# Optimization experiments

Measured on AMD Instinct MI355X. Metric: run time of the kernel, lower is better.

Reference implementation:

```python
import jax, jax.numpy as jnp
import numpy as np
from jax import lax


def setup_inputs() -> dict:
    key = jax.random.key(0)
    k1, k2 = jax.random.split(key)
    B, C, H, W = 4, 32, 512, 512
    x = jax.random.normal(k1, (B, C, H, W), dtype=jnp.float32)
    # offset conv params: out_ch = 2*k*k = 18 (init: small weights, zero bias)
    w_off = jax.random.normal(k2, (18, C, 3, 3), dtype=jnp.float32) * 0.05
    b_off = jnp.zeros((18,), dtype=jnp.float32)
    return {"x": x, "w_off": w_off, "b_off": b_off}


def _grid_sample_bilinear_zeros(x, grid):
    # x: (B,C,H,W); grid: (B,H,W,2) in [-1,1], align_corners=True, zeros padding
    B, C, H, W = x.shape
    ix = (grid[..., 0] + 1.0) * 0.5 * (W - 1)  # (B,H,W)
    iy = (grid[..., 1] + 1.0) * 0.5 * (H - 1)
    x0 = jnp.floor(ix); y0 = jnp.floor(iy)
    x1 = x0 + 1.0;      y1 = y0 + 1.0
    wx1 = ix - x0; wx0 = 1.0 - wx1
    wy1 = iy - y0; wy0 = 1.0 - wy1
    bi = jnp.arange(B)[:, None, None]

    def corner(yc, xc, w):
        valid = (xc >= 0) & (xc <= W - 1) & (yc >= 0) & (yc <= H - 1)
        xi = jnp.clip(xc, 0, W - 1).astype(jnp.int32)
        yi = jnp.clip(yc, 0, H - 1).astype(jnp.int32)
        v = x[bi, :, yi, xi]  # (B,H,W,C)
        return v * (w * valid.astype(x.dtype))[..., None]

    out = (corner(y0, x0, wy0 * wx0) + corner(y0, x1, wy0 * wx1)
           + corner(y1, x0, wy1 * wx0) + corner(y1, x1, wy1 * wx1))
    return out.transpose(0, 3, 1, 2)  # (B,C,H,W)


def reference(x, w_off, b_off):
    B, C, H, W = x.shape
    # offset conv: 3x3, stride 1, padding 1 (shape-preserving)
    off = lax.conv_general_dilated(
        x, w_off, window_strides=(1, 1), padding=((1, 1), (1, 1)),
        dimension_numbers=("NCHW", "OIHW", "NCHW"))
    off = off + b_off[None, :, None, None]               # (B,18,H,W)
    off = off.transpose(0, 2, 3, 1).reshape(B, H, W, 9, 2)
    # base integer grid: (x, y) per pixel
    gy, gx = jnp.meshgrid(jnp.arange(H, dtype=x.dtype),
                          jnp.arange(W, dtype=x.dtype), indexing="ij")
    base = jnp.stack([gx, gy], axis=-1)                  # (H,W,2)
    g = base[None, :, :, None, :] + off                  # (B,H,W,9,2)
    g = g / jnp.array([W - 1, H - 1], dtype=x.dtype) * 2.0 - 1.0
    g = g[:, :, :, 0, :]                                 # only first kernel offset used
    return _grid_sample_bilinear_zeros(x, g)
```

## Files before the change

### kernel.cpp

```cpp
#include <hip/hip_runtime.h>

#define BB 4
#define CC 32
#define HH 512
#define WW 512
#define PLANE ((size_t)HH * WW)
#define NPIX ((size_t)BB * HH * WW)

__global__ __launch_bounds__(256) void conv_off_kernel(
    const float* __restrict__ x, const float* __restrict__ w_off,
    const float* __restrict__ b_off, float* __restrict__ off) {
  const int nb = gridDim.x;
  const int i  = blockIdx.x;
  const int j  = (i & 7) * (nb >> 3) + (i >> 3);
  const int b    = j >> 7;
  const int row0 = (j & 127) << 2;

  const int t  = threadIdx.x;
  const int w4 = (t & 127) << 2;
  const int h0 = row0 + ((t >> 7) << 1);

  float4 a0v, a1v, b0v, b1v;
  {
    const float b0 = b_off[0], b1 = b_off[1];
    a0v.x = a0v.y = a0v.z = a0v.w = b0;  b0v = a0v;
    a1v.x = a1v.y = a1v.z = a1v.w = b1;  b1v = a1v;
  }

  const float* xb = x + (size_t)b * CC * PLANE + (size_t)h0 * WW + w4;
  const float* wp0 = w_off;
  const float* wp1 = w_off + 288;

  for (int ci = 0; ci < CC; ++ci) {
    float vl[4], vr[4], v0[4], v1[4], v2[4], v3[4];
#pragma unroll
    for (int r = 0; r < 4; ++r) {
      const int hy = h0 - 1 + r;
      if (hy >= 0 && hy < HH) {
        const float* p = xb + (ptrdiff_t)(r - 1) * WW;
        const float4 m = *(const float4*)p;
        vl[r] = (w4 > 0) ? p[-1] : 0.f;
        vr[r] = (w4 < WW - 4) ? p[4] : 0.f;
        v0[r] = m.x; v1[r] = m.y; v2[r] = m.z; v3[r] = m.w;
      } else {
        vl[r] = vr[r] = v0[r] = v1[r] = v2[r] = v3[r] = 0.f;
      }
    }
#pragma unroll
    for (int kh = 0; kh < 3; ++kh) {
      const float a0 = wp0[kh * 3 + 0], a1 = wp0[kh * 3 + 1], a2 = wp0[kh * 3 + 2];
      const float c0 = wp1[kh * 3 + 0], c1 = wp1[kh * 3 + 1], c2 = wp1[kh * 3 + 2];
      {
        const int r = kh;
        a0v.x += vl[r] * a0 + v0[r] * a1 + v1[r] * a2;
        a0v.y += v0[r] * a0 + v1[r] * a1 + v2[r] * a2;
        a0v.z += v1[r] * a0 + v2[r] * a1 + v3[r] * a2;
        a0v.w += v2[r] * a0 + v3[r] * a1 + vr[r] * a2;
        a1v.x += vl[r] * c0 + v0[r] * c1 + v1[r] * c2;
        a1v.y += v0[r] * c0 + v1[r] * c1 + v2[r] * c2;
        a1v.z += v1[r] * c0 + v2[r] * c1 + v3[r] * c2;
        a1v.w += v2[r] * c0 + v3[r] * c1 + vr[r] * c2;
      }
      {
        const int r = kh + 1;
        b0v.x += vl[r] * a0 + v0[r] * a1 + v1[r] * a2;
        b0v.y += v0[r] * a0 + v1[r] * a1 + v2[r] * a2;
        b0v.z += v1[r] * a0 + v2[r] * a1 + v3[r] * a2;
        b0v.w += v2[r] * a0 + v3[r] * a1 + vr[r] * a2;
        b1v.x += vl[r] * c0 + v0[r] * c1 + v1[r] * c2;
        b1v.y += v0[r] * c0 + v1[r] * c1 + v2[r] * c2;
        b1v.z += v1[r] * c0 + v2[r] * c1 + v3[r] * c2;
        b1v.w += v2[r] * c0 + v3[r] * c1 + vr[r] * c2;
      }
    }
    wp0 += 9;
    wp1 += 9;
    xb += PLANE;
  }

  const size_t idx = ((size_t)b * HH + h0) * WW + w4;
  *(float4*)(off + idx) = a0v;
  *(float4*)(off + idx + WW) = b0v;
  *(float4*)(off + NPIX + idx) = a1v;
  *(float4*)(off + NPIX + idx + WW) = b1v;
}

__global__ __launch_bounds__(256) void sample_kernel(
    const float* __restrict__ x, const float* __restrict__ off,
    float* __restrict__ out) {
  const int nb = gridDim.x;
  const int i  = blockIdx.x;
  const int j  = (i & 7) * (nb >> 3) + (i >> 3);
  const size_t tid = (size_t)j * 256 + threadIdx.x;

  const int w = (int)(tid & (WW - 1));
  const int h = (int)((tid >> 9) & (HH - 1));
  const int b = (int)(tid >> 18);

  const float ix = (float)w + off[tid];
  const float iy = (float)h + off[NPIX + tid];

  const float x0f = floorf(ix);
  const float y0f = floorf(iy);

  const float wx1 = ix - x0f;
  const float wx0 = 1.f - wx1;
  const float wy1 = iy - y0f;
  const float wy0 = 1.f - wy1;

  const bool vx0 = (x0f >= 0.f) && (x0f <= (float)(WW - 1));
  const bool vx1 = (x0f + 1.f >= 0.f) && (x0f + 1.f <= (float)(WW - 1));
  const bool vy0 = (y0f >= 0.f) && (y0f <= (float)(HH - 1));
  const bool vy1 = (y0f + 1.f >= 0.f) && (y0f + 1.f <= (float)(HH - 1));

  const int xi0 = (int)fminf(fmaxf(x0f, 0.f), (float)(WW - 1));
  const int xi1 = (int)fminf(fmaxf(x0f + 1.f, 0.f), (float)(WW - 1));
  const int yi0 = (int)fminf(fmaxf(y0f, 0.f), (float)(HH - 1));
  const int yi1 = (int)fminf(fmaxf(y0f + 1.f, 0.f), (float)(HH - 1));

  const float w00 = wy0 * wx0 * ((vy0 && vx0) ? 1.f : 0.f);
  const float w01 = wy0 * wx1 * ((vy0 && vx1) ? 1.f : 0.f);
  const float w10 = wy1 * wx0 * ((vy1 && vx0) ? 1.f : 0.f);
  const float w11 = wy1 * wx1 * ((vy1 && vx1) ? 1.f : 0.f);

  const int i00 = yi0 * WW + xi0;
  const int i01 = yi0 * WW + xi1;
  const int i10 = yi1 * WW + xi0;
  const int i11 = yi1 * WW + xi1;

  const float* xp = x + (size_t)b * CC * PLANE;
  float* ob = out + (size_t)b * CC * PLANE + (size_t)h * WW + w;

#pragma unroll 8
  for (int c = 0; c < CC; ++c) {
    const float v = w00 * xp[i00] + w01 * xp[i01] + w10 * xp[i10] + w11 * xp[i11];
    __builtin_nontemporal_store(v, ob);
    xp += PLANE;
    ob += PLANE;
  }
}

extern "C" void kernel_launch(void* const* d_in, const int* in_sizes, int n_in,
                              void* d_out, int out_size, void* d_ws, size_t ws_size,
                              hipStream_t stream) {
  const float* x     = (const float*)d_in[0];
  const float* w_off = (const float*)d_in[1];
  const float* b_off = (const float*)d_in[2];
  float* out = (float*)d_out;
  float* off = (float*)d_ws;

  conv_off_kernel<<<512, 256, 0, stream>>>(x, w_off, b_off, off);

  const int nblk = (int)(NPIX / 256);
  sample_kernel<<<nblk, 256, 0, stream>>>(x, off, out);
}
```

Measured before the change: 339.1 us.

## Compute one output row per thread with double-buffered channel loads in offset conv

Each thread in the offset convolution now produces one output row instead of two, and the grid doubles to 1024 blocks to cover the same work. The channel loop is software-pipelined: the next channel's three input rows are loaded into a second register buffer while the current channel is being accumulated, to hide global load latency. Each thread carries fewer accumulators, but each input row is now loaded by up to three threads instead of being shared across two output rows, so global and cache traffic rises.

New measurement: 331.6 us. 1.02x faster.

```diff
diff --git a/kernel.cpp b/kernel.cpp
--- a/kernel.cpp
+++ b/kernel.cpp
@@ -13,76 +13,70 @@
   const int nb = gridDim.x;
   const int i  = blockIdx.x;
   const int j  = (i & 7) * (nb >> 3) + (i >> 3);
-  const int b    = j >> 7;
-  const int row0 = (j & 127) << 2;
+  const int b    = j >> 8;
+  const int row0 = (j & 255) << 1;
 
   const int t  = threadIdx.x;
   const int w4 = (t & 127) << 2;
-  const int h0 = row0 + ((t >> 7) << 1);
+  const int h  = row0 + (t >> 7);
 
-  float4 a0v, a1v, b0v, b1v;
-  {
-    const float b0 = b_off[0], b1 = b_off[1];
-    a0v.x = a0v.y = a0v.z = a0v.w = b0;  b0v = a0v;
-    a1v.x = a1v.y = a1v.z = a1v.w = b1;  b1v = a1v;
-  }
+  float4 a0v, a1v;
+  a0v.x = a0v.y = a0v.z = a0v.w = b_off[0];
+  a1v.x = a1v.y = a1v.z = a1v.w = b_off[1];
 
-  const float* xb = x + (size_t)b * CC * PLANE + (size_t)h0 * WW + w4;
-  const float* wp0 = w_off;
-  const float* wp1 = w_off + 288;
+  const float* xb = x + (size_t)b * CC * PLANE + (size_t)h * WW + w4;
 
-  for (int ci = 0; ci < CC; ++ci) {
-    float vl[4], vr[4], v0[4], v1[4], v2[4], v3[4];
+  float4 mA[3], mB[3];
+  float vlA[3], vrA[3], vlB[3], vrB[3];
+
+  auto load_ch = [&](int ci, float4* m, float* vl, float* vr) {
 #pragma unroll
-    for (int r = 0; r < 4; ++r) {
-      const int hy = h0 - 1 + r;
+    for (int r = 0; r < 3; ++r) {
+      const int hy = h - 1 + r;
       if (hy >= 0 && hy < HH) {
-        const float* p = xb + (ptrdiff_t)(r - 1) * WW;
-        const float4 m = *(const float4*)p;
-        vl[r] = (w4 > 0) ? p[-1] : 0.f;
-        vr[r] = (w4 < WW - 4) ? p[4] : 0.f;
-        v0[r] = m.x; v1[r] = m.y; v2[r] = m.z; v3[r] = m.w;
+        const float* q = xb + (size_t)ci * PLANE + (ptrdiff_t)(r - 1) * WW;
+        m[r] = *(const float4*)q;
+        vl[r] = (w4 > 0) ? q[-1] : 0.f;
+        vr[r] = (w4 < WW - 4) ? q[4] : 0.f;
       } else {
-        vl[r] = vr[r] = v0[r] = v1[r] = v2[r] = v3[r] = 0.f;
+        m[r].x = m[r].y = m[r].z = m[r].w = 0.f;
+        vl[r] = vr[r] = 0.f;
       }
     }
+  };
+
+  auto compute_ch = [&](int ci, const float4* m, const float* vl, const float* vr) {
+    const float* wp0 = w_off + ci * 9;
+    const float* wp1 = w_off + 288 + ci * 9;
 #pragma unroll
     for (int kh = 0; kh < 3; ++kh) {
       const float a0 = wp0[kh * 3 + 0], a1 = wp0[kh * 3 + 1], a2 = wp0[kh * 3 + 2];
       const float c0 = wp1[kh * 3 + 0], c1 = wp1[kh * 3 + 1], c2 = wp1[kh * 3 + 2];
-      {
-        const int r = kh;
-        a0v.x += vl[r] * a0 + v0[r] * a1 + v1[r] * a2;
-        a0v.y += v0[r] * a0 + v1[r] * a1 + v2[r] * a2;
-        a0v.z += v1[r] * a0 + v2[r] * a1 + v3[r] * a2;
-        a0v.w += v2[r] * a0 + v3[r] * a1 + vr[r] * a2;
-        a1v.x += vl[r] * c0 + v0[r] * c1 + v1[r] * c2;
-        a1v.y += v0[r] * c0 + v1[r] * c1 + v2[r] * c2;
-        a1v.z += v1[r] * c0 + v2[r] * c1 + v3[r] * c2;
-        a1v.w += v2[r] * c0 + v3[r] * c1 + vr[r] * c2;
-      }
-      {
-        const int r = kh + 1;
-        b0v.x += vl[r] * a0 + v0[r] * a1 + v1[r] * a2;
-        b0v.y += v0[r] * a0 + v1[r] * a1 + v2[r] * a2;
-        b0v.z += v1[r] * a0 + v2[r] * a1 + v3[r] * a2;
-        b0v.w += v2[r] * a0 + v3[r] * a1 + vr[r] * a2;
-        b1v.x += vl[r] * c0 + v0[r] * c1 + v1[r] * c2;
-        b1v.y += v0[r] * c0 + v1[r] * c1 + v2[r] * c2;
-        b1v.z += v1[r] * c0 + v2[r] * c1 + v3[r] * c2;
-        b1v.w += v2[r] * c0 + v3[r] * c1 + vr[r] * c2;
-      }
+      a0v.x += vl[kh] * a0 + m[kh].x * a1 + m[kh].y * a2;
+      a0v.y += m[kh].x * a0 + m[kh].y * a1 + m[kh].z * a2;
+      a0v.z += m[kh].y * a0 + m[kh].z * a1 + m[kh].w * a2;
+      a0v.w += m[kh].z * a0 + m[kh].w * a1 + vr[kh] * a2;
+      a1v.x += vl[kh] * c0 + m[kh].x * c1 + m[kh].y * c2;
+      a1v.y += m[kh].x * c0 + m[kh].y * c1 + m[kh].z * c2;
+      a1v.z += m[kh].y * c0 + m[kh].z * c1 + m[kh].w * c2;
+      a1v.w += m[kh].z * c0 + m[kh].w * c1 + vr[kh] * c2;
     }
-    wp0 += 9;
-    wp1 += 9;
-    xb += PLANE;
+  };
+
+  load_ch(0, mA, vlA, vrA);
+  for (int ci = 0; ci < CC - 2; ci += 2) {
+    load_ch(ci + 1, mB, vlB, vrB);
+    compute_ch(ci, mA, vlA, vrA);
+    load_ch(ci + 2, mA, vlA, vrA);
+    compute_ch(ci + 1, mB, vlB, vrB);
   }
+  load_ch(CC - 1, mB, vlB, vrB);
+  compute_ch(CC - 2, mA, vlA, vrA);
+  compute_ch(CC - 1, mB, vlB, vrB);
 
-  const size_t idx = ((size_t)b * HH + h0) * WW + w4;
+  const size_t idx = ((size_t)b * HH + h) * WW + w4;
   *(float4*)(off + idx) = a0v;
-  *(float4*)(off + idx + WW) = b0v;
   *(float4*)(off + NPIX + idx) = a1v;
-  *(float4*)(off + NPIX + idx + WW) = b1v;
 }
 
 __global__ __launch_bounds__(256) void sample_kernel(
@@ -149,7 +143,7 @@
   float* out = (float*)d_out;
   float* off = (float*)d_ws;
 
-  conv_off_kernel<<<512, 256, 0, stream>>>(x, w_off, b_off, off);
+  conv_off_kernel<<<1024, 256, 0, stream>>>(x, w_off, b_off, off);
 
   const int nblk = (int)(NPIX / 256);
   sample_kernel<<<nblk, 256, 0, stream>>>(x, off, out);
```
